# Kernel tuning notes

Hardware: AMD Instinct MI355X
Metric: run time of the kernel (lower is better)

The kernel has to match this reference:

```python
import jax, jax.numpy as jnp
import numpy as np

B, S, HID = 1, 2048, 2048
H = 16
D_NOPE, D_ROPE, D_V = 128, 64, 128
Q_HEAD = D_NOPE + D_ROPE  # 192
QL, KVL = 1536, 512
EPS = 1e-6
SCALE = Q_HEAD ** -0.5


def rms_norm(x, w, eps=EPS):
    return x * jax.lax.rsqrt(jnp.mean(x * x, axis=-1, keepdims=True) + eps) * w


def rotate_half(x):
    h = x.shape[-1] // 2
    return jnp.concatenate([-x[..., h:], x[..., :h]], axis=-1)


def apply_rope(x, cos, sin):
    # DeepSeek de-interleave: view(..., d//2, 2).transpose(-1,-2).reshape == [even, odd]
    x = jnp.concatenate([x[..., 0::2], x[..., 1::2]], axis=-1)
    return x * cos + rotate_half(x) * sin


def setup_inputs() -> dict:
    key = jax.random.key(0)
    ks = jax.random.split(key, 8)
    x = jax.random.normal(ks[0], (B, S, HID), dtype=jnp.float32)
    # causal additive mask
    causal = jnp.tril(jnp.ones((S, S), dtype=bool))
    mask = jnp.where(causal, 0.0, -1e9).astype(jnp.float32)[None, None]
    position_ids = jnp.broadcast_to(jnp.arange(S, dtype=jnp.int32), (B, S))
    # RoPE caches, theta=10000
    inv_freq = 1.0 / (10000.0 ** (np.arange(0, D_ROPE, 2, dtype=np.float32) / D_ROPE))
    freqs = np.outer(np.arange(S, dtype=np.float32), inv_freq)
    emb = np.concatenate([freqs, freqs], axis=-1)
    cos = jnp.asarray(np.cos(emb), dtype=jnp.float32)
    sin = jnp.asarray(np.sin(emb), dtype=jnp.float32)
    w = lambda k, shp: (jax.random.normal(k, shp, dtype=jnp.float32) * 0.02)
    return {
        "x": x, "mask": mask, "position_ids": position_ids, "cos": cos, "sin": sin,
        "q_a_w": w(ks[1], (HID, QL)),
        "q_a_ln": jnp.ones((QL,), jnp.float32),
        "q_b_w": w(ks[2], (QL, H * Q_HEAD)),
        "kv_a_w": w(ks[3], (HID, KVL + D_ROPE)),
        "kv_a_ln": jnp.ones((KVL,), jnp.float32),
        "kv_b_w": w(ks[4], (KVL, H * (D_NOPE + D_V))),
        "o_w": w(ks[5], (H * D_V, HID)),
    }


def reference(x, mask, position_ids, cos, sin, q_a_w, q_a_ln, q_b_w, kv_a_w, kv_a_ln, kv_b_w, o_w):
    b, s, _ = x.shape
    # low-rank Q projection
    q = rms_norm(x @ q_a_w, q_a_ln) @ q_b_w            # [B,S,H*192]
    q = q.reshape(b, s, H, Q_HEAD).transpose(0, 2, 1, 3)  # [B,H,S,192]
    q_nope, q_pe = q[..., :D_NOPE], q[..., D_NOPE:]
    # compressed KV + decoupled rope key (MQA, shared across heads)
    ckv = x @ kv_a_w                                   # [B,S,512+64]
    c_norm = rms_norm(ckv[..., :KVL], kv_a_ln)         # [B,S,512]
    k_pe = ckv[..., KVL:][:, None]                     # [B,1,S,64]
    kv = (c_norm @ kv_b_w).reshape(b, s, H, D_NOPE + D_V).transpose(0, 2, 1, 3)
    k_nope, value = kv[..., :D_NOPE], kv[..., D_NOPE:]  # [B,H,S,128] each
    # rope
    cos_p = cos[position_ids][:, None]                 # [B,1,S,64]
    sin_p = sin[position_ids][:, None]
    q_pe = apply_rope(q_pe, cos_p, sin_p)
    k_pe = apply_rope(k_pe, cos_p, sin_p)
    query = jnp.concatenate([q_nope, q_pe], axis=-1)   # [B,H,S,192]
    key = jnp.concatenate([k_nope, jnp.broadcast_to(k_pe, (b, H, s, D_ROPE))], axis=-1)
    scores = jnp.einsum("bhsd,bhtd->bhst", query, key) * SCALE + mask
    attn = jax.nn.softmax(scores, axis=-1)
    out = jnp.einsum("bhst,bhtd->bhsd", attn, value)   # [B,H,S,128]
    out = out.transpose(0, 2, 1, 3).reshape(b, s, H * D_V) @ o_w
    kv_cache = jnp.concatenate([c_norm, k_pe[:, 0]], axis=-1)  # [B,S,576] latent cache
    return out, kv_cache
```

## Files before the change

### kernel.cpp

```cpp
#include <hip/hip_runtime.h>

typedef unsigned short u16;
typedef __bf16 bf16x8 __attribute__((ext_vector_type(8)));
typedef short s16x4 __attribute__((ext_vector_type(4)));
typedef short s16x8 __attribute__((ext_vector_type(8)));
typedef float f32x4 __attribute__((ext_vector_type(4)));

#define S_LEN 2048
#define NHEAD 16
#define QHEAD 192
#define EPS 1e-6f
#define ATTN_SCALE 0.07216878364870323f
#define QSCALE_LOG2E 0.10412011228586118f

__device__ __forceinline__ u16 f2bf(float f) {
    unsigned u = __builtin_bit_cast(unsigned, f);
    u = (u + 0x7FFFu + ((u >> 16) & 1u)) >> 16;
    return (u16)u;
}
__device__ __forceinline__ float bf2f(u16 h) {
    unsigned u = ((unsigned)h) << 16;
    return __builtin_bit_cast(float, u);
}

__device__ __forceinline__ void gl_lds16(const u16* g, u16* l) {
    __builtin_amdgcn_global_load_lds(
        (const __attribute__((address_space(1))) unsigned int*)g,
        (__attribute__((address_space(3))) unsigned int*)l,
        16, 0, 0);
}

#if defined(__has_builtin) && __has_builtin(__builtin_amdgcn_mfma_f32_16x16x16bf16_1k)
__device__ __forceinline__ f32x4 mfma16(s16x4 a, s16x4 b, f32x4 c) {
    return __builtin_amdgcn_mfma_f32_16x16x16bf16_1k(a, b, c, 0, 0, 0);
}
#else
__device__ __forceinline__ f32x4 mfma16(s16x4 a, s16x4 b, f32x4 c) {
    asm volatile("v_mfma_f32_16x16x16_bf16 %0, %1, %2, %0"
                 : "+v"(c) : "v"(a), "v"(b));
    return c;
}
#endif

template <int CF32>
__device__ __forceinline__ void gemm_core(
    u16* __restrict__ smem,
    const u16* __restrict__ A, const u16* __restrict__ B, void* __restrict__ Cv,
    int K, int lda, int ldb, int ldc, int tm, int tn)
{
    const int tid = threadIdx.x;
    const int w = tid >> 6, lane = tid & 63;
    const int q = lane >> 4, r = lane & 15;

    const int lr = lane & 15;
    const int lc = (lane >> 4) * 8;
    const u16* ga0 = A + (long)(tm * 128 + w * 32 + lr) * lda + lc;
    const u16* ga1 = ga0 + 16 * (long)lda;
    const u16* gb0 = B + (long)(tn * 128 + w * 32 + lr) * ldb + lc;
    const u16* gb1 = gb0 + 16 * (long)ldb;
    const int sa0 = w * 1024, sa1 = sa0 + 512;
    const int sb0 = 4096 + w * 1024, sb1 = sb0 + 512;

    f32x4 acc[4][4] = {};
    const int wm = w >> 1;
    const int wn = w & 1;
    const int n = K >> 6;

    gl_lds16(ga0, smem + sa0);
    gl_lds16(ga1, smem + sa1);
    gl_lds16(gb0, smem + sb0);
    gl_lds16(gb1, smem + sb1);
    gl_lds16(ga0 + 32, smem + 8192 + sa0);
    gl_lds16(ga1 + 32, smem + 8192 + sa1);
    gl_lds16(gb0 + 32, smem + 8192 + sb0);
    gl_lds16(gb1 + 32, smem + 8192 + sb1);
    asm volatile("s_waitcnt vmcnt(0)" ::: "memory");
    __builtin_amdgcn_sched_barrier(0);
    __builtin_amdgcn_s_barrier();
    __builtin_amdgcn_sched_barrier(0);

    for (int t = 0; t < n; ++t) {
        u16* const cur = smem + (t & 1) * 16384;
        u16* const nxt = smem + ((t + 1) & 1) * 16384;
        if (t + 1 < n) {
            const long k1 = (long)(t + 1) << 6;
            gl_lds16(ga0 + k1, nxt + sa0);
            gl_lds16(ga1 + k1, nxt + sa1);
            gl_lds16(gb0 + k1, nxt + sb0);
            gl_lds16(gb1 + k1, nxt + sb1);
            gl_lds16(ga0 + k1 + 32, nxt + 8192 + sa0);
            gl_lds16(ga1 + k1 + 32, nxt + 8192 + sa1);
            gl_lds16(gb0 + k1 + 32, nxt + 8192 + sb0);
            gl_lds16(gb1 + k1 + 32, nxt + 8192 + sb1);
        }
        #pragma unroll
        for (int kk = 0; kk < 2; ++kk) {
            u16* const sub = cur + kk * 8192;
            bf16x8 af[4], bv[4];
            #pragma unroll
            for (int mt = 0; mt < 4; ++mt)
                af[mt] = *(const bf16x8*)&sub[(wm * 4 + mt) * 512 + lane * 8];
            #pragma unroll
            for (int nt = 0; nt < 4; ++nt)
                bv[nt] = *(const bf16x8*)&sub[4096 + (wn * 4 + nt) * 512 + lane * 8];
            #pragma unroll
            for (int mt = 0; mt < 4; ++mt)
                #pragma unroll
                for (int nt = 0; nt < 4; ++nt)
                    acc[mt][nt] = __builtin_amdgcn_mfma_f32_16x16x32_bf16(
                        af[mt], bv[nt], acc[mt][nt], 0, 0, 0);
        }
        if (t + 1 < n) {
            asm volatile("s_waitcnt vmcnt(0)" ::: "memory");
            __builtin_amdgcn_sched_barrier(0);
            __builtin_amdgcn_s_barrier();
            __builtin_amdgcn_sched_barrier(0);
        }
    }

    const int row0 = tm * 128 + wm * 64 + q * 4;
    const int col0 = tn * 128 + wn * 64 + r;
    if (CF32) {
        float* C = (float*)Cv;
        #pragma unroll
        for (int mt = 0; mt < 4; ++mt)
            #pragma unroll
            for (int i = 0; i < 4; ++i) {
                long rb = (long)(row0 + mt * 16 + i) * ldc + col0;
                #pragma unroll
                for (int nt = 0; nt < 4; ++nt)
                    C[rb + nt * 16] = acc[mt][nt][i];
            }
    } else {
        u16* C = (u16*)Cv;
        #pragma unroll
        for (int mt = 0; mt < 4; ++mt)
            #pragma unroll
            for (int i = 0; i < 4; ++i) {
                long rb = (long)(row0 + mt * 16 + i) * ldc + col0;
                #pragma unroll
                for (int nt = 0; nt < 4; ++nt)
                    C[rb + nt * 16] = f2bf(acc[mt][nt][i]);
            }
    }
}

template <int CF32>
__global__ __launch_bounds__(256, 2)
void gemm_bt(const u16* __restrict__ A, const u16* __restrict__ B,
             void* __restrict__ Cv, int K, int lda, int ldb, int ldc)
{
    __shared__ __align__(16) u16 smem[2 * 16384];
    gemm_core<CF32>(smem, A, B, Cv, K, lda, ldb, ldc, blockIdx.y, blockIdx.x);
}

__global__ __launch_bounds__(256, 2)
void gemm_bt_dual(const u16* __restrict__ A0, const u16* __restrict__ B0,
                  void* __restrict__ C0, int K0, int lda0, int ldb0, int ldc0, int nx0,
                  const u16* __restrict__ A1, const u16* __restrict__ B1,
                  void* __restrict__ C1, int K1, int lda1, int ldb1, int ldc1, int nx1)
{
    __shared__ __align__(16) u16 smem[2 * 16384];
    if (blockIdx.z == 0) {
        if ((int)blockIdx.x >= nx0) return;
        gemm_core<0>(smem, A0, B0, C0, K0, lda0, ldb0, ldc0, blockIdx.y, blockIdx.x);
    } else {
        if ((int)blockIdx.x >= nx1) return;
        gemm_core<0>(smem, A1, B1, C1, K1, lda1, ldb1, ldc1, blockIdx.y, blockIdx.x);
    }
}

template<int C0, int C1>
__device__ __forceinline__ void stage_tile(
    const u16* __restrict__ kvb, const u16* __restrict__ kpe,
    const u16* __restrict__ vt,
    u16* __restrict__ Kl, u16* __restrict__ Vl,
    int h, int t, int quad, int r)
{
    #pragma unroll
    for (int c = C0; c < C1; ++c) {
        if (c < 24) {
            const int mtk = c / 6, kc = c % 6;
            const int row = t * 64 + mtk * 16 + r;
            const u16* src = (kc < 4)
                ? kvb + (size_t)row * 4096 + h * 256 + kc * 32 + quad * 8
                : kpe + (size_t)row * 64 + (kc - 4) * 32 + quad * 8;
            gl_lds16(src, &Kl[c * 512]);
        } else {
            const int cv = c - 24, mtd = cv >> 1, sc = cv & 1;
            const u16* src = vt + ((size_t)h * 128 + mtd * 16 + r) * 2048
                             + t * 64 + sc * 32 + quad * 8;
            gl_lds16(src, &Vl[cv * 512]);
        }
    }
}

__device__ __forceinline__ void stage_dispatch(
    const u16* __restrict__ kvb, const u16* __restrict__ kpe,
    const u16* __restrict__ vt,
    u16* __restrict__ Kl, u16* __restrict__ Vl,
    int w, int h, int t, int quad, int r)
{
    if (w == 0)      stage_tile<0, 10>(kvb, kpe, vt, Kl, Vl, h, t, quad, r);
    else if (w == 1) stage_tile<10, 20>(kvb, kpe, vt, Kl, Vl, h, t, quad, r);
    else if (w == 2) stage_tile<20, 30>(kvb, kpe, vt, Kl, Vl, h, t, quad, r);
    else             stage_tile<30, 40>(kvb, kpe, vt, Kl, Vl, h, t, quad, r);
}

__device__ __forceinline__ void kv_tile_step(
    const u16* __restrict__ Kl, const u16* __restrict__ Vl,
    const bf16x8 (&Qf)[6], f32x4 (&Oacc)[8], float& lsum,
    int lane, int quad, int r, int kglob0, int qg, bool maskT)
{
    f32x4 Sacc[4];
    #pragma unroll
    for (int mtk = 0; mtk < 4; ++mtk)
        Sacc[mtk] = (f32x4){0.f, 0.f, 0.f, 0.f};
    #pragma unroll
    for (int kc = 0; kc < 6; ++kc)
        #pragma unroll
        for (int mtk = 0; mtk < 4; ++mtk) {
            bf16x8 Ak = *(const bf16x8*)&Kl[(mtk * 6 + kc) * 512 + lane * 8];
            Sacc[mtk] = __builtin_amdgcn_mfma_f32_16x16x32_bf16(
                Ak, Qf[kc], Sacc[mtk], 0, 0, 0);
        }
    #pragma unroll
    for (int sc = 0; sc < 2; ++sc) {
        s16x4 Pf[2];
        #pragma unroll
        for (int half = 0; half < 2; ++half) {
            const int kb = sc * 2 + half;
            const int kb0 = kglob0 + kb * 16 + quad * 4;
            #pragma unroll
            for (int i = 0; i < 4; ++i) {
                float pv = exp2f(Sacc[kb][i]);
                if (maskT && (kb0 + i > qg)) pv = 0.f;
                lsum += pv;
                Pf[half][i] = (short)f2bf(pv);
            }
        }
        #pragma unroll
        for (int mtd = 0; mtd < 8; ++mtd) {
            s16x8 Av8 = *(const s16x8*)&Vl[(mtd * 2 + sc) * 512 + quad * 128 + r * 8];
            s16x4 lo = __builtin_shufflevector(Av8, Av8, 0, 1, 2, 3);
            s16x4 hi = __builtin_shufflevector(Av8, Av8, 4, 5, 6, 7);
            Oacc[mtd] = mfma16(lo, Pf[0], Oacc[mtd]);
            Oacc[mtd] = mfma16(hi, Pf[1], Oacc[mtd]);
        }
    }
}

__global__ __launch_bounds__(256, 2)
void flash_attn(const u16* __restrict__ query, const u16* __restrict__ kvb,
                const u16* __restrict__ kpe, const u16* __restrict__ vt,
                u16* __restrict__ ao)
{
    const int tid = threadIdx.x;
    const int w = tid >> 6, lane = tid & 63;
    const int quad = lane >> 4, r = lane & 15;

    const int bid = (int)blockIdx.x;
    const int i = bid & 255;
    const int t_ = i >> 4;
    const int h = i & 15;
    const int j = (bid < 256) ? (31 - t_) : t_;

    const int q0 = j * 64;
    const int ntk = j + 1;

    __shared__ __align__(16) u16 smem[40960];

    const int qg = q0 + w * 16 + r;

    bf16x8 Qf[6];
    #pragma unroll
    for (int kc = 0; kc < 6; ++kc)
        Qf[kc] = *(const bf16x8*)(query
            + ((size_t)h * S_LEN + q0 + w * 16 + r) * QHEAD
            + kc * 32 + quad * 8);

    f32x4 Oacc[8];
    #pragma unroll
    for (int mtd = 0; mtd < 8; ++mtd)
        Oacc[mtd] = (f32x4){0.f, 0.f, 0.f, 0.f};
    float lsum = 0.f;

    stage_dispatch(kvb, kpe, vt, smem, smem + 12288, w, h, 0, quad, r);
    __syncthreads();

    for (int t = 0; t < ntk; ++t) {
        u16* const curb = smem + (t & 1) * 20480;
        u16* const nxtb = smem + ((t + 1) & 1) * 20480;
        if (t + 1 < ntk)
            stage_dispatch(kvb, kpe, vt, nxtb, nxtb + 12288, w, h, t + 1, quad, r);
        kv_tile_step(curb, curb + 12288, Qf, Oacc, lsum,
                     lane, quad, r, t * 64, qg, t == ntk - 1);
        __syncthreads();
    }

    float l = lsum;
    l += __shfl_xor(l, 16, 64);
    l += __shfl_xor(l, 32, 64);
    const float inv = 1.0f / l;
    const int qrow = q0 + w * 16 + r;
    #pragma unroll
    for (int mtd = 0; mtd < 8; ++mtd) {
        ushort4 o;
        o.x = f2bf(Oacc[mtd][0] * inv);
        o.y = f2bf(Oacc[mtd][1] * inv);
        o.z = f2bf(Oacc[mtd][2] * inv);
        o.w = f2bf(Oacc[mtd][3] * inv);
        *(ushort4*)(ao + (size_t)qrow * 2048 + h * 128 + mtd * 16 + quad * 4) = o;
    }
}

__device__ __forceinline__ void wtrans_body(
    float (*tile)[33], const float* __restrict__ in, u16* __restrict__ out,
    int K, int N, int bx, int by, int tid)
{
    const int tx = tid & 31, ty = tid >> 5;
    const int k0 = bx * 32, n0 = by * 32;
    #pragma unroll
    for (int jj = 0; jj < 32; jj += 8) {
        int nn = n0 + tx;
        tile[ty + jj][tx] = (nn < N) ? in[(long)(k0 + ty + jj) * N + nn] : 0.0f;
    }
    __syncthreads();
    #pragma unroll
    for (int jj = 0; jj < 32; jj += 8)
        out[(long)(n0 + ty + jj) * K + k0 + tx] = f2bf(tile[tx][ty + jj]);
}

__global__ __launch_bounds__(256)
void prep_k(const float4* __restrict__ x4, ushort4* __restrict__ xb4,
            const float* __restrict__ q_a_w, const float* __restrict__ kv_a_w,
            const float* __restrict__ q_b_w, const float* __restrict__ kv_b_w,
            const float* __restrict__ o_w,
            u16* __restrict__ W1, u16* __restrict__ qbwt,
            u16* __restrict__ kvbwt, u16* __restrict__ owt)
{
    __shared__ float tile[32][33];
    const int tid = threadIdx.x;
    int b = (int)blockIdx.x;
    if (b < 4096) {
        int i = b * 256 + tid;
        float4 v = x4[i];
        ushort4 o;
        o.x = f2bf(v.x); o.y = f2bf(v.y); o.z = f2bf(v.z); o.w = f2bf(v.w);
        xb4[i] = o;
        return;
    }
    b -= 4096;
    if (b < 3072)       wtrans_body(tile, q_a_w,  W1,                  2048, 1536, b % 64, b / 64, tid);
    else if ((b -= 3072) < 1280) wtrans_body(tile, kv_a_w, W1 + 1536ULL * 2048, 2048, 576,  b % 64, b / 64, tid);
    else if ((b -= 1280) < 4608) wtrans_body(tile, q_b_w,  qbwt,       1536, 3072, b % 48, b / 48, tid);
    else if ((b -= 4608) < 2048) wtrans_body(tile, kv_b_w, kvbwt,      512,  4096, b % 16, b / 16, tid);
    else { b -= 2048;            wtrans_body(tile, o_w,    owt,        2048, 2048, b % 64, b / 64, tid); }
}

__global__ __launch_bounds__(256)
void norm_k(u16* __restrict__ qkv, const float* __restrict__ q_ln,
            const float* __restrict__ kv_ln, const int* __restrict__ pos_ids,
            const float* __restrict__ cosb, const float* __restrict__ sinb,
            float* __restrict__ kvout, u16* __restrict__ cnb,
            u16* __restrict__ kpe)
{
    const int s = blockIdx.x, tid = threadIdx.x;
    u16* row = qkv + (long)s * 2176;
    u16* row2 = row + 1536;
    __shared__ float red[8];
    float sum = 0.f;
    for (int d = tid; d < 1536; d += 256) { float v = bf2f(row[d]); sum += v * v; }
    #pragma unroll
    for (int o = 32; o; o >>= 1) sum += __shfl_xor(sum, o, 64);
    if ((tid & 63) == 0) red[tid >> 6] = sum;
    float sum2 = 0.f;
    for (int d = tid; d < 512; d += 256) { float v = bf2f(row2[d]); sum2 += v * v; }
    #pragma unroll
    for (int o = 32; o; o >>= 1) sum2 += __shfl_xor(sum2, o, 64);
    if ((tid & 63) == 0) red[4 + (tid >> 6)] = sum2;
    __syncthreads();
    sum  = red[0] + red[1] + red[2] + red[3];
    sum2 = red[4] + red[5] + red[6] + red[7];
    const float sc1 = rsqrtf(sum / 1536.f + EPS);
    const float sc2 = rsqrtf(sum2 / 512.f + EPS);
    for (int d = tid; d < 1536; d += 256)
        row[d] = f2bf(bf2f(row[d]) * sc1 * q_ln[d]);
    for (int d = tid; d < 512; d += 256) {
        float v = bf2f(row2[d]) * sc2 * kv_ln[d];
        kvout[(long)s * 576 + d] = v;
        cnb[(long)s * 512 + d] = f2bf(v);
    }
    if (tid < 32) {
        int p = pos_ids[s];
        float x0 = bf2f(row2[512 + 2 * tid]);
        float x1 = bf2f(row2[512 + 2 * tid + 1]);
        float c1 = cosb[p * 64 + tid], s1 = sinb[p * 64 + tid];
        float c2 = cosb[p * 64 + 32 + tid], s2 = sinb[p * 64 + 32 + tid];
        float lo = x0 * c1 - x1 * s1;
        float hi = x1 * c2 + x0 * s2;
        kvout[(long)s * 576 + 512 + tid] = lo;
        kvout[(long)s * 576 + 544 + tid] = hi;
        kpe[(long)s * 64 + tid] = f2bf(lo);
        kpe[(long)s * 64 + 32 + tid] = f2bf(hi);
    }
}

__global__ __launch_bounds__(256)
void post_k(const u16* __restrict__ qb, const int* __restrict__ pos_ids,
            const float* __restrict__ cosb, const float* __restrict__ sinb,
            u16* __restrict__ query, const u16* __restrict__ kv,
            u16* __restrict__ vt)
{
    __shared__ u16 tile[32][33];
    const int tid = threadIdx.x;
    int b = (int)blockIdx.x;
    if (b < 2048) {
        const int s = b;
        const u16* row = qb + (long)s * 3072;
        {
            int h = tid >> 4, c = tid & 15;
            const u16* src = &row[h * QHEAD + c * 8];
            u16* dst = &query[((long)(h * S_LEN + s)) * QHEAD + c * 8];
            ushort4 a = *(const ushort4*)src;
            ushort4 bb = *(const ushort4*)(src + 4);
            ushort4 oa, ob;
            oa.x = f2bf(bf2f(a.x) * QSCALE_LOG2E); oa.y = f2bf(bf2f(a.y) * QSCALE_LOG2E);
            oa.z = f2bf(bf2f(a.z) * QSCALE_LOG2E); oa.w = f2bf(bf2f(a.w) * QSCALE_LOG2E);
            ob.x = f2bf(bf2f(bb.x) * QSCALE_LOG2E); ob.y = f2bf(bf2f(bb.y) * QSCALE_LOG2E);
            ob.z = f2bf(bf2f(bb.z) * QSCALE_LOG2E); ob.w = f2bf(bf2f(bb.w) * QSCALE_LOG2E);
            *(ushort4*)dst = oa;
            *(ushort4*)(dst + 4) = ob;
        }
        int p = pos_ids[s];
        for (int idx = tid; idx < 512; idx += 256) {
            int h = idx >> 5, i = idx & 31;
            float x0 = bf2f(row[h * QHEAD + 128 + 2 * i]);
            float x1 = bf2f(row[h * QHEAD + 128 + 2 * i + 1]);
            float c1 = cosb[p * 64 + i], s1 = sinb[p * 64 + i];
            float c2 = cosb[p * 64 + 32 + i], s2 = sinb[p * 64 + 32 + i];
            u16* qr = query + ((long)(h * S_LEN + s)) * QHEAD;
            qr[128 + i] = f2bf((x0 * c1 - x1 * s1) * QSCALE_LOG2E);
            qr[160 + i] = f2bf((x1 * c2 + x0 * s2) * QSCALE_LOG2E);
        }
    } else {
        b -= 2048;
        const int s0 = (b & 63) * 32, d0 = ((b >> 6) & 3) * 32, h = b >> 8;
        const int tx = tid & 31, ty = tid >> 5;
        #pragma unroll
        for (int jj = 0; jj < 32; jj += 8)
            tile[ty + jj][tx] = kv[(long)(s0 + ty + jj) * 4096 + h * 256 + 128 + d0 + tx];
        __syncthreads();
        const int txp = ((tx >> 2) & 3) * 8 + (tx >> 4) * 4 + (tx & 3);
        #pragma unroll
        for (int jj = 0; jj < 32; jj += 8)
            vt[(long)(h * 128 + d0 + ty + jj) * S_LEN + s0 + txp] = tile[tx][ty + jj];
    }
}

extern "C" void kernel_launch(void* const* d_in, const int* in_sizes, int n_in,
                              void* d_out, int out_size, void* d_ws, size_t ws_size,
                              hipStream_t stream)
{
    const float* x      = (const float*)d_in[0];
    const int*   posid  = (const int*)d_in[2];
    const float* cosb   = (const float*)d_in[3];
    const float* sinb   = (const float*)d_in[4];
    const float* q_a_w  = (const float*)d_in[5];
    const float* q_a_ln = (const float*)d_in[6];
    const float* q_b_w  = (const float*)d_in[7];
    const float* kv_a_w = (const float*)d_in[8];
    const float* kv_a_ln= (const float*)d_in[9];
    const float* kv_b_w = (const float*)d_in[10];
    const float* o_w    = (const float*)d_in[11];

    float* out    = (float*)d_out;
    float* kv_out = out + (size_t)2048 * 2048;

    char* ws = (char*)d_ws;
    size_t off = 0;
    auto alloc = [&](size_t bytes) { char* p = ws + off; off += (bytes + 255) & ~(size_t)255; return p; };
    u16* xb    = (u16*)alloc(2048ULL * 2048 * 2);
    u16* W1    = (u16*)alloc(2176ULL * 2048 * 2);
    u16* qbwt  = (u16*)alloc(3072ULL * 1536 * 2);
    u16* kvbwt = (u16*)alloc(4096ULL * 512 * 2);
    u16* owt   = (u16*)alloc(2048ULL * 2048 * 2);
    u16* qkv_a = (u16*)alloc(2048ULL * 2176 * 2);
    u16* qbuf  = (u16*)alloc(2048ULL * 3072 * 2);
    u16* query = (u16*)alloc(16ULL * 2048 * 192 * 2);
    u16* cnb   = (u16*)alloc(2048ULL * 512 * 2);
    u16* kpe   = (u16*)alloc(2048ULL * 64 * 2);
    u16* kvbuf = (u16*)alloc(2048ULL * 4096 * 2);
    u16* vt    = (u16*)alloc(16ULL * 128 * 2048 * 2);
    u16* ao    = (u16*)alloc(2048ULL * 2048 * 2);
    (void)ws_size; (void)in_sizes; (void)n_in; (void)out_size;

    dim3 blk(256);

    prep_k<<<dim3(19200), blk, 0, stream>>>(
        (const float4*)x, (ushort4*)xb, q_a_w, kv_a_w, q_b_w, kv_b_w, o_w,
        W1, qbwt, kvbwt, owt);

    gemm_bt<0><<<dim3(17, 16), blk, 0, stream>>>(xb, W1, qkv_a, 2048, 2048, 2048, 2176);

    norm_k<<<dim3(2048), blk, 0, stream>>>(qkv_a, q_a_ln, kv_a_ln, posid,
                                           cosb, sinb, kv_out, cnb, kpe);

    gemm_bt_dual<<<dim3(32, 16, 2), blk, 0, stream>>>(
        qkv_a, qbwt, qbuf, 1536, 2176, 1536, 3072, 24,
        cnb, kvbwt, kvbuf, 512, 512, 512, 4096, 32);

    post_k<<<dim3(6144), blk, 0, stream>>>(qbuf, posid, cosb, sinb, query, kvbuf, vt);

    flash_attn<<<dim3(512), dim3(256), 0, stream>>>(query, kvbuf, kpe, vt, ao);

    gemm_bt<1><<<dim3(16, 16), blk, 0, stream>>>(ao, owt, out, 2048, 2048, 2048, 2048);
}
```

Baseline: 395.3 us.

## Split-K the input and output projection GEMMs with fp32 partial reduction

The first projection GEMM and the output GEMM now split K in two along blockIdx.z, doubling the block count so the 256 CUs are better filled. Each half writes fp32 partials into workspace reused from buffers not yet live. For the first GEMM, norm_k sums the two partials into a shared-memory row before RMS norm and RoPE. For the output GEMM, a new elementwise kernel adds the partial into the output. The trade is extra fp32 partial write and read traffic, one more launch, and reliance on reused buffers spilling into adjacent free regions.

```diff
diff --git a/kernel.cpp b/kernel.cpp
--- a/kernel.cpp
+++ b/kernel.cpp
@@ -145,13 +145,16 @@
     }
 }
 
-template <int CF32>
 __global__ __launch_bounds__(256, 2)
-void gemm_bt(const u16* __restrict__ A, const u16* __restrict__ B,
-             void* __restrict__ Cv, int K, int lda, int ldb, int ldc)
+void gemm_ks(const u16* __restrict__ A, const u16* __restrict__ B,
+             float* __restrict__ C0, float* __restrict__ C1,
+             int Kh, int lda, int ldb, int ldc)
 {
     __shared__ __align__(16) u16 smem[2 * 16384];
-    gemm_core<CF32>(smem, A, B, Cv, K, lda, ldb, ldc, blockIdx.y, blockIdx.x);
+    const int z = blockIdx.z;
+    float* C = z ? C1 : C0;
+    gemm_core<1>(smem, A + (long)z * Kh, B + (long)z * Kh, C,
+                 Kh, lda, ldb, ldc, blockIdx.y, blockIdx.x);
 }
 
 __global__ __launch_bounds__(256, 2)
@@ -163,11 +166,22 @@
     __shared__ __align__(16) u16 smem[2 * 16384];
     if (blockIdx.z == 0) {
         if ((int)blockIdx.x >= nx0) return;
-        gemm_core<0>(smem, A0, B0, C0, K0, lda0, ldb0, ldc0, blockIdx.y, blockIdx.x);
+        gemm_core<0>(smem, A0, B0, C0, K0, lda0, ldb0, ldc0,
+                     blockIdx.y, blockIdx.x);
     } else {
         if ((int)blockIdx.x >= nx1) return;
-        gemm_core<0>(smem, A1, B1, C1, K1, lda1, ldb1, ldc1, blockIdx.y, blockIdx.x);
-    }
+        gemm_core<0>(smem, A1, B1, C1, K1, lda1, ldb1, ldc1,
+                     blockIdx.y, blockIdx.x);
+    }
+}
+
+__global__ __launch_bounds__(256)
+void addout_k(float4* __restrict__ out, const float4* __restrict__ p)
+{
+    int i = blockIdx.x * 256 + threadIdx.x;
+    float4 a = out[i], b = p[i];
+    a.x += b.x; a.y += b.y; a.z += b.z; a.w += b.w;
+    out[i] = a;
 }
 
 template<int C0, int C1>
@@ -359,42 +373,46 @@
 }
 
 __global__ __launch_bounds__(256)
-void norm_k(u16* __restrict__ qkv, const float* __restrict__ q_ln,
+void norm_k(const float* __restrict__ pa, const float* __restrict__ pb,
+            u16* __restrict__ qkv, const float* __restrict__ q_ln,
             const float* __restrict__ kv_ln, const int* __restrict__ pos_ids,
             const float* __restrict__ cosb, const float* __restrict__ sinb,
             float* __restrict__ kvout, u16* __restrict__ cnb,
             u16* __restrict__ kpe)
 {
     const int s = blockIdx.x, tid = threadIdx.x;
-    u16* row = qkv + (long)s * 2176;
-    u16* row2 = row + 1536;
+    __shared__ float rowbuf[2176];
     __shared__ float red[8];
-    float sum = 0.f;
-    for (int d = tid; d < 1536; d += 256) { float v = bf2f(row[d]); sum += v * v; }
-    #pragma unroll
-    for (int o = 32; o; o >>= 1) sum += __shfl_xor(sum, o, 64);
-    if ((tid & 63) == 0) red[tid >> 6] = sum;
-    float sum2 = 0.f;
-    for (int d = tid; d < 512; d += 256) { float v = bf2f(row2[d]); sum2 += v * v; }
-    #pragma unroll
-    for (int o = 32; o; o >>= 1) sum2 += __shfl_xor(sum2, o, 64);
-    if ((tid & 63) == 0) red[4 + (tid >> 6)] = sum2;
+    const long base = (long)s * 2176;
+    float sum1 = 0.f, sum2 = 0.f;
+    for (int d = tid; d < 2176; d += 256) {
+        float v = pa[base + d] + pb[base + d];
+        rowbuf[d] = v;
+        if (d < 1536)      sum1 += v * v;
+        else if (d < 2048) sum2 += v * v;
+    }
+    #pragma unroll
+    for (int o = 32; o; o >>= 1) {
+        sum1 += __shfl_xor(sum1, o, 64);
+        sum2 += __shfl_xor(sum2, o, 64);
+    }
+    if ((tid & 63) == 0) { red[tid >> 6] = sum1; red[4 + (tid >> 6)] = sum2; }
     __syncthreads();
-    sum  = red[0] + red[1] + red[2] + red[3];
+    sum1 = red[0] + red[1] + red[2] + red[3];
     sum2 = red[4] + red[5] + red[6] + red[7];
-    const float sc1 = rsqrtf(sum / 1536.f + EPS);
+    const float sc1 = rsqrtf(sum1 / 1536.f + EPS);
     const float sc2 = rsqrtf(sum2 / 512.f + EPS);
     for (int d = tid; d < 1536; d += 256)
-        row[d] = f2bf(bf2f(row[d]) * sc1 * q_ln[d]);
+        qkv[base + d] = f2bf(rowbuf[d] * sc1 * q_ln[d]);
     for (int d = tid; d < 512; d += 256) {
-        float v = bf2f(row2[d]) * sc2 * kv_ln[d];
+        float v = rowbuf[1536 + d] * sc2 * kv_ln[d];
         kvout[(long)s * 576 + d] = v;
         cnb[(long)s * 512 + d] = f2bf(v);
     }
     if (tid < 32) {
         int p = pos_ids[s];
-        float x0 = bf2f(row2[512 + 2 * tid]);
-        float x1 = bf2f(row2[512 + 2 * tid + 1]);
+        float x0 = rowbuf[2048 + 2 * tid];
+        float x1 = rowbuf[2048 + 2 * tid + 1];
         float c1 = cosb[p * 64 + tid], s1 = sinb[p * 64 + tid];
         float c2 = cosb[p * 64 + 32 + tid], s2 = sinb[p * 64 + 32 + tid];
         float lo = x0 * c1 - x1 * s1;
@@ -495,16 +513,21 @@
     u16* ao    = (u16*)alloc(2048ULL * 2048 * 2);
     (void)ws_size; (void)in_sizes; (void)n_in; (void)out_size;
 
+    float* g1p0 = (float*)qbuf;
+    float* g1p1 = (float*)kvbuf;
+    float* g5p  = (float*)xb;
+
     dim3 blk(256);
 
     prep_k<<<dim3(19200), blk, 0, stream>>>(
         (const float4*)x, (ushort4*)xb, q_a_w, kv_a_w, q_b_w, kv_b_w, o_w,
         W1, qbwt, kvbwt, owt);
 
-    gemm_bt<0><<<dim3(17, 16), blk, 0, stream>>>(xb, W1, qkv_a, 2048, 2048, 2048, 2176);
-
-    norm_k<<<dim3(2048), blk, 0, stream>>>(qkv_a, q_a_ln, kv_a_ln, posid,
-                                           cosb, sinb, kv_out, cnb, kpe);
+    gemm_ks<<<dim3(17, 16, 2), blk, 0, stream>>>(
+        xb, W1, g1p0, g1p1, 1024, 2048, 2048, 2176);
+
+    norm_k<<<dim3(2048), blk, 0, stream>>>(g1p0, g1p1, qkv_a, q_a_ln, kv_a_ln,
+                                           posid, cosb, sinb, kv_out, cnb, kpe);
 
     gemm_bt_dual<<<dim3(32, 16, 2), blk, 0, stream>>>(
         qkv_a, qbwt, qbuf, 1536, 2176, 1536, 3072, 24,
@@ -514,5 +537,7 @@
 
     flash_attn<<<dim3(512), dim3(256), 0, stream>>>(query, kvbuf, kpe, vt, ao);
 
-    gemm_bt<1><<<dim3(16, 16), blk, 0, stream>>>(ao, owt, out, 2048, 2048, 2048, 2048);
-}
+    gemm_ks<<<dim3(16, 16, 2), blk, 0, stream>>>(
+        ao, owt, g5p, out, 1024, 2048, 2048, 2048);
+    addout_k<<<dim3(4096), blk, 0, stream>>>((float4*)out, (const float4*)g5p);
+}
```

New measurement: 390.6 us. No clear change (-1.2%).
